# Kernel tuning notes

Measured on AMD Instinct MI355X. Metric: run time of the kernel, lower is better.

Reference implementation:

```python
import jax, jax.numpy as jnp
import numpy as np

VOCAB = 50257
HID = 1024


def setup_inputs() -> dict:
    key = jax.random.key(0)
    ks = jax.random.split(key, 9)
    s = 0.05  # weight scale for numerical sanity
    return {
        "input": jax.random.randint(ks[0], (1,), 0, VOCAB),
        "hidden": jax.random.normal(ks[1], (1, 1, HID), jnp.float32),
        "emb": jax.random.normal(ks[2], (VOCAB, HID), jnp.float32) * s,
        "w_ih": jax.random.normal(ks[3], (3 * HID, HID), jnp.float32) * s,
        "w_hh": jax.random.normal(ks[4], (3 * HID, HID), jnp.float32) * s,
        "b_ih": jax.random.normal(ks[5], (3 * HID,), jnp.float32) * s,
        "b_hh": jax.random.normal(ks[6], (3 * HID,), jnp.float32) * s,
        "w_out": jax.random.normal(ks[7], (VOCAB, HID), jnp.float32) * s,
        "b_out": jax.random.normal(ks[8], (VOCAB,), jnp.float32) * s,
    }


def reference(input, hidden, emb, w_ih, w_hh, b_ih, b_hh, w_out, b_out):
    # embedding lookup -> [1, HID], then ReLU
    x = jnp.maximum(emb[input[0]], 0.0)[None, :]          # [1, H]
    h = hidden[0]                                         # [1, H] (layer 0)
    # PyTorch GRU cell, gate order (r, z, n)
    gi = x @ w_ih.T + b_ih                                # [1, 3H]
    gh = h @ w_hh.T + b_hh                                # [1, 3H]
    i_r, i_z, i_n = jnp.split(gi, 3, axis=1)
    h_r, h_z, h_n = jnp.split(gh, 3, axis=1)
    r = jax.nn.sigmoid(i_r + h_r)
    z = jax.nn.sigmoid(i_z + h_z)
    n = jnp.tanh(i_n + r * h_n)
    h_new = (1.0 - z) * n + z * h                         # [1, H]
    # output projection + log-softmax over vocab (dim=1)
    logits = h_new @ w_out.T + b_out                      # [1, V]
    out = jax.nn.log_softmax(logits, axis=1)
    return out, h_new[None, :, :]
```

## Files before the change

kernel.cpp:

```cpp
#include <hip/hip_runtime.h>
#include <hip/hip_bf16.h>
#include <math.h>

#define HID   1024
#define HID3  3072
#define VOCAB 50257

#define LROWS   16
#define LBLOCKS ((VOCAB + LROWS - 1) / LROWS)

#define FBLOCKS 32

#define WS_GI   0
#define WS_GH   3072
#define WS_PSUM 6144

typedef float f32x4 __attribute__((ext_vector_type(4)));

__device__ __forceinline__ float wave_reduce_sum(float s) {
    #pragma unroll
    for (int off = 32; off; off >>= 1) s += __shfl_down(s, off, 64);
    return s;
}

__device__ __forceinline__ float dot4(f32x4 a, f32x4 b) {
    return a.x * b.x + a.y * b.y + a.z * b.z + a.w * b.w;
}

__global__ void gates_kernel(const int* __restrict__ token,
                             const float* __restrict__ emb,
                             const float* __restrict__ w_ih,
                             const float* __restrict__ w_hh,
                             const float* __restrict__ b_ih,
                             const float* __restrict__ b_hh,
                             const float* __restrict__ h,
                             float* __restrict__ gi,
                             float* __restrict__ gh) {
    int gwave = (blockIdx.x * blockDim.x + threadIdx.x) >> 6;
    int lane  = threadIdx.x & 63;
    bool isI  = gwave < HID3;
    int row   = isI ? gwave : gwave - HID3;
    const f32x4* w = (const f32x4*)((isI ? w_ih : w_hh) + (size_t)row * HID);

    f32x4 w0 = w[lane];
    f32x4 w1 = w[64 + lane];
    f32x4 w2 = w[128 + lane];
    f32x4 w3 = w[192 + lane];

    const f32x4* v = (const f32x4*)(isI ? (emb + (size_t)token[0] * HID) : h);
    f32x4 v0 = v[lane];
    f32x4 v1 = v[64 + lane];
    f32x4 v2 = v[128 + lane];
    f32x4 v3 = v[192 + lane];
    if (isI) {
        v0.x=fmaxf(v0.x,0.f); v0.y=fmaxf(v0.y,0.f); v0.z=fmaxf(v0.z,0.f); v0.w=fmaxf(v0.w,0.f);
        v1.x=fmaxf(v1.x,0.f); v1.y=fmaxf(v1.y,0.f); v1.z=fmaxf(v1.z,0.f); v1.w=fmaxf(v1.w,0.f);
        v2.x=fmaxf(v2.x,0.f); v2.y=fmaxf(v2.y,0.f); v2.z=fmaxf(v2.z,0.f); v2.w=fmaxf(v2.w,0.f);
        v3.x=fmaxf(v3.x,0.f); v3.y=fmaxf(v3.y,0.f); v3.z=fmaxf(v3.z,0.f); v3.w=fmaxf(v3.w,0.f);
    }

    float s = dot4(w0, v0) + dot4(w1, v1) + dot4(w2, v2) + dot4(w3, v3);
    s = wave_reduce_sum(s);
    if (lane == 0) {
        if (isI) gi[row] = s + b_ih[row];
        else     gh[row] = s + b_hh[row];
    }
}

__global__ void logits_kernel(const float* __restrict__ gi,
                              const float* __restrict__ gh,
                              const float* __restrict__ h,
                              const float* __restrict__ w_out,
                              const float* __restrict__ b_out,
                              float* __restrict__ out,
                              float* __restrict__ hn_out,
                              float* __restrict__ psum) {
    __shared__ float lh[HID];
    __shared__ float wsum[8];
    int t = threadIdx.x, lane = t & 63, w = t >> 6;

    int r0 = blockIdx.x * LROWS + w * 2;
    int r1 = r0 + 1;
    int c0 = r0 < VOCAB ? r0 : VOCAB - 1;
    int c1 = r1 < VOCAB ? r1 : VOCAB - 1;
    const f32x4* wa = (const f32x4*)(w_out + (size_t)c0 * HID);
    const f32x4* wb = (const f32x4*)(w_out + (size_t)c1 * HID);

    f32x4 a0 = wa[lane], a1 = wa[64 + lane], a2 = wa[128 + lane], a3 = wa[192 + lane];
    f32x4 b0 = wb[lane], b1 = wb[64 + lane], b2 = wb[128 + lane], b3 = wb[192 + lane];

    #pragma unroll
    for (int e = 0; e < 2; ++e) {
        int j = t + e * 512;
        float r = 1.0f / (1.0f + expf(-(gi[j] + gh[j])));
        float z = 1.0f / (1.0f + expf(-(gi[HID + j] + gh[HID + j])));
        float n = tanhf(gi[2 * HID + j] + r * gh[2 * HID + j]);
        float hn = (1.0f - z) * n + z * h[j];
        lh[j] = hn;
        if (blockIdx.x == 0) hn_out[j] = hn;
    }
    __syncthreads();

    const f32x4* lhv = (const f32x4*)lh;
    f32x4 h0 = lhv[lane], h1 = lhv[64 + lane], h2 = lhv[128 + lane], h3 = lhv[192 + lane];

    float s0 = dot4(a0, h0) + dot4(a1, h1) + dot4(a2, h2) + dot4(a3, h3);
    float s1 = dot4(b0, h0) + dot4(b1, h1) + dot4(b2, h2) + dot4(b3, h3);
    s0 = wave_reduce_sum(s0);
    s1 = wave_reduce_sum(s1);
    if (lane == 0) {
        float e = 0.0f;
        if (r0 < VOCAB) { float l0 = s0 + b_out[r0]; out[r0] = l0; e += expf(l0); }
        if (r1 < VOCAB) { float l1 = s1 + b_out[r1]; out[r1] = l1; e += expf(l1); }
        wsum[w] = e;
    }
    __syncthreads();
    if (t == 0) {
        float tot = 0.0f;
        #pragma unroll
        for (int i = 0; i < 8; ++i) tot += wsum[i];
        psum[blockIdx.x] = tot;
    }
}

__global__ void finish_kernel(const float* __restrict__ psum,
                              float* __restrict__ out) {
    __shared__ float wred[8];
    int t = threadIdx.x, lane = t & 63, w = t >> 6;

    float s = 0.0f;
    for (int i = t; i < LBLOCKS; i += 512) s += psum[i];
    s = wave_reduce_sum(s);
    if (lane == 0) wred[w] = s;
    __syncthreads();
    float tot = 0.0f;
    #pragma unroll
    for (int i = 0; i < 8; ++i) tot += wred[i];
    float lse = logf(tot);

    int i4 = (blockIdx.x * 512 + t) * 4;
    if (i4 + 3 < VOCAB) {
        f32x4 v = *(const f32x4*)(out + i4);
        v.x -= lse; v.y -= lse; v.z -= lse; v.w -= lse;
        *(f32x4*)(out + i4) = v;
    } else if (i4 < VOCAB) {
        for (int k = 0; k < 4; ++k)
            if (i4 + k < VOCAB) out[i4 + k] -= lse;
    }
}

extern "C" void kernel_launch(void* const* d_in, const int* in_sizes, int n_in,
                              void* d_out, int out_size, void* d_ws, size_t ws_size,
                              hipStream_t stream) {
    const int*   token = (const int*)  d_in[0];
    const float* hidden= (const float*)d_in[1];
    const float* emb   = (const float*)d_in[2];
    const float* w_ih  = (const float*)d_in[3];
    const float* w_hh  = (const float*)d_in[4];
    const float* b_ih  = (const float*)d_in[5];
    const float* b_hh  = (const float*)d_in[6];
    const float* w_out = (const float*)d_in[7];
    const float* b_out = (const float*)d_in[8];

    float* ws  = (float*)d_ws;
    float* out = (float*)d_out;

    float* ws_gi = ws + WS_GI;
    float* ws_gh = ws + WS_GH;
    float* ws_ps = ws + WS_PSUM;

    gates_kernel<<<768, 512, 0, stream>>>(token, emb, w_ih, w_hh, b_ih, b_hh,
                                          hidden, ws_gi, ws_gh);

    logits_kernel<<<LBLOCKS, 512, 0, stream>>>(ws_gi, ws_gh, hidden,
                                               w_out, b_out,
                                               out, out + VOCAB, ws_ps);

    finish_kernel<<<FBLOCKS, 512, 0, stream>>>(ws_ps, out);
}
```

Before: 46.26 us.

## Fuse GRU gates, logits and log-softmax into one cooperative persistent kernel

```diff
diff --git a/kernel.cpp b/kernel.cpp
--- a/kernel.cpp
+++ b/kernel.cpp
@@ -1,15 +1,16 @@
 #include <hip/hip_runtime.h>
-#include <hip/hip_bf16.h>
+#include <hip/hip_cooperative_groups.h>
 #include <math.h>
 
-#define HID   1024
-#define HID3  3072
-#define VOCAB 50257
+namespace cg = cooperative_groups;
 
-#define LROWS   16
-#define LBLOCKS ((VOCAB + LROWS - 1) / LROWS)
+#define HID    1024
+#define HID3   3072
+#define VOCAB  50257
 
-#define FBLOCKS 32
+#define NBLK   512
+#define NTHR   512
+#define LGROUPS ((VOCAB + 15) / 16)
 
 #define WS_GI   0
 #define WS_GH   3072
@@ -27,126 +28,112 @@
     return a.x * b.x + a.y * b.y + a.z * b.z + a.w * b.w;
 }
 
-__global__ void gates_kernel(const int* __restrict__ token,
-                             const float* __restrict__ emb,
-                             const float* __restrict__ w_ih,
-                             const float* __restrict__ w_hh,
-                             const float* __restrict__ b_ih,
-                             const float* __restrict__ b_hh,
-                             const float* __restrict__ h,
-                             float* __restrict__ gi,
-                             float* __restrict__ gh) {
-    int gwave = (blockIdx.x * blockDim.x + threadIdx.x) >> 6;
-    int lane  = threadIdx.x & 63;
-    bool isI  = gwave < HID3;
-    int row   = isI ? gwave : gwave - HID3;
-    const f32x4* w = (const f32x4*)((isI ? w_ih : w_hh) + (size_t)row * HID);
+__global__ __launch_bounds__(NTHR, 4) void fused_kernel(
+        const int*   __restrict__ token,
+        const float* __restrict__ emb,
+        const float* __restrict__ w_ih,
+        const float* __restrict__ w_hh,
+        const float* __restrict__ b_ih,
+        const float* __restrict__ b_hh,
+        const float* __restrict__ h,
+        const float* __restrict__ w_out,
+        const float* __restrict__ b_out,
+        float* __restrict__ gi,
+        float* __restrict__ gh,
+        float* __restrict__ psum,
+        float* __restrict__ out,
+        float* __restrict__ hn_out) {
+    cg::grid_group grid = cg::this_grid();
+    __shared__ float lh[HID];
+    __shared__ float wsum[8];
+    __shared__ float wred[8];
 
-    f32x4 w0 = w[lane];
-    f32x4 w1 = w[64 + lane];
-    f32x4 w2 = w[128 + lane];
-    f32x4 w3 = w[192 + lane];
+    int t = threadIdx.x, lane = t & 63, w = t >> 6, b = blockIdx.x;
 
-    const f32x4* v = (const f32x4*)(isI ? (emb + (size_t)token[0] * HID) : h);
-    f32x4 v0 = v[lane];
-    f32x4 v1 = v[64 + lane];
-    f32x4 v2 = v[128 + lane];
-    f32x4 v3 = v[192 + lane];
-    if (isI) {
-        v0.x=fmaxf(v0.x,0.f); v0.y=fmaxf(v0.y,0.f); v0.z=fmaxf(v0.z,0.f); v0.w=fmaxf(v0.w,0.f);
-        v1.x=fmaxf(v1.x,0.f); v1.y=fmaxf(v1.y,0.f); v1.z=fmaxf(v1.z,0.f); v1.w=fmaxf(v1.w,0.f);
-        v2.x=fmaxf(v2.x,0.f); v2.y=fmaxf(v2.y,0.f); v2.z=fmaxf(v2.z,0.f); v2.w=fmaxf(v2.w,0.f);
-        v3.x=fmaxf(v3.x,0.f); v3.y=fmaxf(v3.y,0.f); v3.z=fmaxf(v3.z,0.f); v3.w=fmaxf(v3.w,0.f);
+    {
+        bool isI = (b < 256);
+        const float* wmat = isI ? w_ih : w_hh;
+        const float* bias = isI ? b_ih : b_hh;
+        float*       gout = isI ? gi   : gh;
+        int rbase = (isI ? b : b - 256) * 12;
+
+        const f32x4* v4 = (const f32x4*)(isI ? (emb + (size_t)token[0] * HID) : h);
+        f32x4 v0 = v4[lane], v1 = v4[64 + lane], v2 = v4[128 + lane], v3 = v4[192 + lane];
+        if (isI) {
+            v0.x=fmaxf(v0.x,0.f); v0.y=fmaxf(v0.y,0.f); v0.z=fmaxf(v0.z,0.f); v0.w=fmaxf(v0.w,0.f);
+            v1.x=fmaxf(v1.x,0.f); v1.y=fmaxf(v1.y,0.f); v1.z=fmaxf(v1.z,0.f); v1.w=fmaxf(v1.w,0.f);
+            v2.x=fmaxf(v2.x,0.f); v2.y=fmaxf(v2.y,0.f); v2.z=fmaxf(v2.z,0.f); v2.w=fmaxf(v2.w,0.f);
+            v3.x=fmaxf(v3.x,0.f); v3.y=fmaxf(v3.y,0.f); v3.z=fmaxf(v3.z,0.f); v3.w=fmaxf(v3.w,0.f);
+        }
+        for (int l = w; l < 12; l += 8) {
+            int row = rbase + l;
+            const f32x4* wr = (const f32x4*)(wmat + (size_t)row * HID);
+            f32x4 w0 = wr[lane], w1 = wr[64 + lane], w2 = wr[128 + lane], w3 = wr[192 + lane];
+            float s = dot4(w0, v0) + dot4(w1, v1) + dot4(w2, v2) + dot4(w3, v3);
+            s = wave_reduce_sum(s);
+            if (lane == 0) gout[row] = s + bias[row];
+        }
     }
 
-    float s = dot4(w0, v0) + dot4(w1, v1) + dot4(w2, v2) + dot4(w3, v3);
-    s = wave_reduce_sum(s);
-    if (lane == 0) {
-        if (isI) gi[row] = s + b_ih[row];
-        else     gh[row] = s + b_hh[row];
-    }
-}
-
-__global__ void logits_kernel(const float* __restrict__ gi,
-                              const float* __restrict__ gh,
-                              const float* __restrict__ h,
-                              const float* __restrict__ w_out,
-                              const float* __restrict__ b_out,
-                              float* __restrict__ out,
-                              float* __restrict__ hn_out,
-                              float* __restrict__ psum) {
-    __shared__ float lh[HID];
-    __shared__ float wsum[8];
-    int t = threadIdx.x, lane = t & 63, w = t >> 6;
-
-    int r0 = blockIdx.x * LROWS + w * 2;
-    int r1 = r0 + 1;
-    int c0 = r0 < VOCAB ? r0 : VOCAB - 1;
-    int c1 = r1 < VOCAB ? r1 : VOCAB - 1;
-    const f32x4* wa = (const f32x4*)(w_out + (size_t)c0 * HID);
-    const f32x4* wb = (const f32x4*)(w_out + (size_t)c1 * HID);
-
-    f32x4 a0 = wa[lane], a1 = wa[64 + lane], a2 = wa[128 + lane], a3 = wa[192 + lane];
-    f32x4 b0 = wb[lane], b1 = wb[64 + lane], b2 = wb[128 + lane], b3 = wb[192 + lane];
+    grid.sync();
 
     #pragma unroll
     for (int e = 0; e < 2; ++e) {
-        int j = t + e * 512;
+        int j = t + e * NTHR;
         float r = 1.0f / (1.0f + expf(-(gi[j] + gh[j])));
         float z = 1.0f / (1.0f + expf(-(gi[HID + j] + gh[HID + j])));
         float n = tanhf(gi[2 * HID + j] + r * gh[2 * HID + j]);
         float hn = (1.0f - z) * n + z * h[j];
         lh[j] = hn;
-        if (blockIdx.x == 0) hn_out[j] = hn;
+        if (b == 0) hn_out[j] = hn;
     }
     __syncthreads();
 
     const f32x4* lhv = (const f32x4*)lh;
     f32x4 h0 = lhv[lane], h1 = lhv[64 + lane], h2 = lhv[128 + lane], h3 = lhv[192 + lane];
 
-    float s0 = dot4(a0, h0) + dot4(a1, h1) + dot4(a2, h2) + dot4(a3, h3);
-    float s1 = dot4(b0, h0) + dot4(b1, h1) + dot4(b2, h2) + dot4(b3, h3);
-    s0 = wave_reduce_sum(s0);
-    s1 = wave_reduce_sum(s1);
-    if (lane == 0) {
-        float e = 0.0f;
-        if (r0 < VOCAB) { float l0 = s0 + b_out[r0]; out[r0] = l0; e += expf(l0); }
-        if (r1 < VOCAB) { float l1 = s1 + b_out[r1]; out[r1] = l1; e += expf(l1); }
-        wsum[w] = e;
+    float eacc = 0.0f;
+    for (int g = b; g < LGROUPS; g += NBLK) {
+        int r0 = g * 16 + w * 2;
+        int r1 = r0 + 1;
+        int c0 = r0 < VOCAB ? r0 : VOCAB - 1;
+        int c1 = r1 < VOCAB ? r1 : VOCAB - 1;
+        const f32x4* wa = (const f32x4*)(w_out + (size_t)c0 * HID);
+        const f32x4* wb = (const f32x4*)(w_out + (size_t)c1 * HID);
+        f32x4 a0 = wa[lane], a1 = wa[64 + lane], a2 = wa[128 + lane], a3 = wa[192 + lane];
+        f32x4 b0 = wb[lane], b1 = wb[64 + lane], b2 = wb[128 + lane], b3 = wb[192 + lane];
+
+        float s0 = dot4(a0, h0) + dot4(a1, h1) + dot4(a2, h2) + dot4(a3, h3);
+        float s1 = dot4(b0, h0) + dot4(b1, h1) + dot4(b2, h2) + dot4(b3, h3);
+        s0 = wave_reduce_sum(s0);
+        s1 = wave_reduce_sum(s1);
+        if (lane == 0) {
+            if (r0 < VOCAB) { float l0 = s0 + b_out[r0]; out[r0] = l0; eacc += expf(l0); }
+            if (r1 < VOCAB) { float l1 = s1 + b_out[r1]; out[r1] = l1; eacc += expf(l1); }
+        }
     }
+    if (lane == 0) wsum[w] = eacc;
     __syncthreads();
     if (t == 0) {
         float tot = 0.0f;
         #pragma unroll
         for (int i = 0; i < 8; ++i) tot += wsum[i];
-        psum[blockIdx.x] = tot;
+        psum[b] = tot;
     }
-}
 
-__global__ void finish_kernel(const float* __restrict__ psum,
-                              float* __restrict__ out) {
-    __shared__ float wred[8];
-    int t = threadIdx.x, lane = t & 63, w = t >> 6;
+    grid.sync();
 
-    float s = 0.0f;
-    for (int i = t; i < LBLOCKS; i += 512) s += psum[i];
-    s = wave_reduce_sum(s);
-    if (lane == 0) wred[w] = s;
+    float p = psum[t];
+    p = wave_reduce_sum(p);
+    if (lane == 0) wred[w] = p;
     __syncthreads();
     float tot = 0.0f;
     #pragma unroll
     for (int i = 0; i < 8; ++i) tot += wred[i];
     float lse = logf(tot);
 
-    int i4 = (blockIdx.x * 512 + t) * 4;
-    if (i4 + 3 < VOCAB) {
-        f32x4 v = *(const f32x4*)(out + i4);
-        v.x -= lse; v.y -= lse; v.z -= lse; v.w -= lse;
-        *(f32x4*)(out + i4) = v;
-    } else if (i4 < VOCAB) {
-        for (int k = 0; k < 4; ++k)
-            if (i4 + k < VOCAB) out[i4 + k] -= lse;
-    }
+    int i = b * NTHR + t;
+    if (i < VOCAB) out[i] -= lse;
 }
 
 extern "C" void kernel_launch(void* const* d_in, const int* in_sizes, int n_in,
@@ -168,13 +155,14 @@
     float* ws_gi = ws + WS_GI;
     float* ws_gh = ws + WS_GH;
     float* ws_ps = ws + WS_PSUM;
+    float* hn_out = out + VOCAB;
 
-    gates_kernel<<<768, 512, 0, stream>>>(token, emb, w_ih, w_hh, b_ih, b_hh,
-                                          hidden, ws_gi, ws_gh);
-
-    logits_kernel<<<LBLOCKS, 512, 0, stream>>>(ws_gi, ws_gh, hidden,
-                                               w_out, b_out,
-                                               out, out + VOCAB, ws_ps);
-
-    finish_kernel<<<FBLOCKS, 512, 0, stream>>>(ws_ps, out);
+    void* args[] = {
+        (void*)&token, (void*)&emb, (void*)&w_ih, (void*)&w_hh,
+        (void*)&b_ih, (void*)&b_hh, (void*)&hidden, (void*)&w_out,
+        (void*)&b_out, (void*)&ws_gi, (void*)&ws_gh, (void*)&ws_ps,
+        (void*)&out, (void*)&hn_out
+    };
+    hipLaunchCooperativeKernel((void*)fused_kernel, dim3(NBLK), dim3(NTHR),
+                               args, 0, stream);
 }
```

After: 144.9 us. 3.13x slower.

## Process 64 vocab rows per logits block with software-prefetched weight loads

Applied to the files above, without the earlier changes.

```diff
diff --git a/kernel.cpp b/kernel.cpp
--- a/kernel.cpp
+++ b/kernel.cpp
@@ -6,9 +6,7 @@
 #define HID3  3072
 #define VOCAB 50257
 
-#define LROWS   16
-#define LBLOCKS ((VOCAB + LROWS - 1) / LROWS)
-
+#define LBLK    786
 #define FBLOCKS 32
 
 #define WS_GI   0
@@ -67,7 +65,19 @@
     }
 }
 
-__global__ void logits_kernel(const float* __restrict__ gi,
+__device__ __forceinline__ void load_pair(const float* __restrict__ w_out,
+                                          int r0, int lane,
+                                          f32x4 A0[4], f32x4 A1[4]) {
+    int c0 = r0 < VOCAB ? r0 : VOCAB - 1;
+    int c1 = r0 + 1 < VOCAB ? r0 + 1 : VOCAB - 1;
+    const f32x4* wa = (const f32x4*)(w_out + (size_t)c0 * HID);
+    const f32x4* wb = (const f32x4*)(w_out + (size_t)c1 * HID);
+    A0[0] = wa[lane]; A0[1] = wa[64 + lane]; A0[2] = wa[128 + lane]; A0[3] = wa[192 + lane];
+    A1[0] = wb[lane]; A1[1] = wb[64 + lane]; A1[2] = wb[128 + lane]; A1[3] = wb[192 + lane];
+}
+
+__global__ __launch_bounds__(512) void logits_kernel(
+                              const float* __restrict__ gi,
                               const float* __restrict__ gh,
                               const float* __restrict__ h,
                               const float* __restrict__ w_out,
@@ -79,15 +89,10 @@
     __shared__ float wsum[8];
     int t = threadIdx.x, lane = t & 63, w = t >> 6;
 
-    int r0 = blockIdx.x * LROWS + w * 2;
-    int r1 = r0 + 1;
-    int c0 = r0 < VOCAB ? r0 : VOCAB - 1;
-    int c1 = r1 < VOCAB ? r1 : VOCAB - 1;
-    const f32x4* wa = (const f32x4*)(w_out + (size_t)c0 * HID);
-    const f32x4* wb = (const f32x4*)(w_out + (size_t)c1 * HID);
+    int rowbase = blockIdx.x * 64 + w * 2;
 
-    f32x4 a0 = wa[lane], a1 = wa[64 + lane], a2 = wa[128 + lane], a3 = wa[192 + lane];
-    f32x4 b0 = wb[lane], b1 = wb[64 + lane], b2 = wb[128 + lane], b3 = wb[192 + lane];
+    f32x4 A0[4], A1[4];
+    load_pair(w_out, rowbase, lane, A0, A1);
 
     #pragma unroll
     for (int e = 0; e < 2; ++e) {
@@ -104,16 +109,28 @@
     const f32x4* lhv = (const f32x4*)lh;
     f32x4 h0 = lhv[lane], h1 = lhv[64 + lane], h2 = lhv[128 + lane], h3 = lhv[192 + lane];
 
-    float s0 = dot4(a0, h0) + dot4(a1, h1) + dot4(a2, h2) + dot4(a3, h3);
-    float s1 = dot4(b0, h0) + dot4(b1, h1) + dot4(b2, h2) + dot4(b3, h3);
-    s0 = wave_reduce_sum(s0);
-    s1 = wave_reduce_sum(s1);
-    if (lane == 0) {
-        float e = 0.0f;
-        if (r0 < VOCAB) { float l0 = s0 + b_out[r0]; out[r0] = l0; e += expf(l0); }
-        if (r1 < VOCAB) { float l1 = s1 + b_out[r1]; out[r1] = l1; e += expf(l1); }
-        wsum[w] = e;
+    float eacc = 0.0f;
+    #pragma unroll
+    for (int k = 0; k < 4; ++k) {
+        f32x4 B0[4], B1[4];
+        if (k < 3) load_pair(w_out, rowbase + (k + 1) * 16, lane, B0, B1);
+
+        float s0 = dot4(A0[0], h0) + dot4(A0[1], h1) + dot4(A0[2], h2) + dot4(A0[3], h3);
+        float s1 = dot4(A1[0], h0) + dot4(A1[1], h1) + dot4(A1[2], h2) + dot4(A1[3], h3);
+        s0 = wave_reduce_sum(s0);
+        s1 = wave_reduce_sum(s1);
+        int r0 = rowbase + k * 16;
+        if (lane == 0) {
+            if (r0 < VOCAB)     { float l0 = s0 + b_out[r0];     out[r0]     = l0; eacc += expf(l0); }
+            if (r0 + 1 < VOCAB) { float l1 = s1 + b_out[r0 + 1]; out[r0 + 1] = l1; eacc += expf(l1); }
+        }
+        if (k < 3) {
+            #pragma unroll
+            for (int i = 0; i < 4; ++i) { A0[i] = B0[i]; A1[i] = B1[i]; }
+        }
     }
+
+    if (lane == 0) wsum[w] = eacc;
     __syncthreads();
     if (t == 0) {
         float tot = 0.0f;
@@ -129,7 +146,7 @@
     int t = threadIdx.x, lane = t & 63, w = t >> 6;
 
     float s = 0.0f;
-    for (int i = t; i < LBLOCKS; i += 512) s += psum[i];
+    for (int i = t; i < LBLK; i += 512) s += psum[i];
     s = wave_reduce_sum(s);
     if (lane == 0) wred[w] = s;
     __syncthreads();
@@ -172,9 +189,9 @@
     gates_kernel<<<768, 512, 0, stream>>>(token, emb, w_ih, w_hh, b_ih, b_hh,
                                           hidden, ws_gi, ws_gh);
 
-    logits_kernel<<<LBLOCKS, 512, 0, stream>>>(ws_gi, ws_gh, hidden,
-                                               w_out, b_out,
-                                               out, out + VOCAB, ws_ps);
+    logits_kernel<<<LBLK, 512, 0, stream>>>(ws_gi, ws_gh, hidden,
+                                            w_out, b_out,
+                                            out, out + VOCAB, ws_ps);
 
     finish_kernel<<<FBLOCKS, 512, 0, stream>>>(ws_ps, out);
 }
```

New measurement: 48.57 us. 1.05x slower.
